# Optimization experiments

Hardware: AMD Instinct MI355X
Metric: run time of the kernel (lower is better)

## Reference

```python
import jax, jax.numpy as jnp
import numpy as np

N_NODES = 50000


def gcn_conv(x, W, b, row, col, n):
    """PyG GCNConv with default add_self_loops=True, normalize=True.
    out[i] = sum_{e: col[e]=i} d^-1/2[row[e]] d^-1/2[i] * (x@W)[row[e]]
             + d^-1[i]*(x@W)[i] + b,  where d = in-degree + 1 (self-loop).
    """
    x_lin = x @ W                                   # [n, out_ch]
    ones = jnp.ones(row.shape[0], dtype=x.dtype)
    deg = jax.ops.segment_sum(ones, col, num_segments=n) + 1.0  # self-loop
    dinv = jax.lax.rsqrt(deg)                       # deg >= 1, safe
    norm = dinv[row] * dinv[col]                    # [E]
    msg = norm[:, None] * x_lin[row]                # [E, out_ch]
    agg = jax.ops.segment_sum(msg, col, num_segments=n)
    self_term = (dinv * dinv)[:, None] * x_lin      # self-loop contribution
    return agg + self_term + b


def setup_inputs() -> dict:
    key = jax.random.key(0)
    ks = jax.random.split(key, 10)
    in_ch, hid, out_ch = 128, 256, 64
    E = 800000
    x = jax.random.normal(ks[0], (N_NODES, in_ch), dtype=jnp.float32)
    edge_attr = jax.random.normal(ks[1], (E, 8), dtype=jnp.float32)  # unused by forward
    edge_index = jax.random.randint(ks[2], (2, E), 0, N_NODES, dtype=jnp.int64)
    def glorot(k, fan_in, fan_out):
        s = float(np.sqrt(6.0 / (fan_in + fan_out)))
        return jax.random.uniform(k, (fan_in, fan_out), jnp.float32, -s, s)
    return {
        "x": x,
        "edge_attr": edge_attr,
        "edge_index": edge_index,
        "W1": glorot(ks[3], in_ch, hid), "b1": jnp.zeros((hid,), jnp.float32),
        "W2": glorot(ks[4], hid, hid),  "b2": jnp.zeros((hid,), jnp.float32),
        "W3": glorot(ks[5], hid, out_ch), "b3": jnp.zeros((out_ch,), jnp.float32),
    }


def reference(x, edge_attr, edge_index, W1, b1, W2, b2, W3, b3):
    n = x.shape[0]
    row, col = edge_index[0], edge_index[1]
    h = jax.nn.sigmoid(gcn_conv(x, W1, b1, row, col, n))
    h = jax.nn.sigmoid(gcn_conv(h, W2, b2, row, col, n))
    # dropout(p=0.1) in eval mode is identity
    return gcn_conv(h, W3, b3, row, col, n)
```

## Files before the change

### kernel.cpp

```cpp
#include <hip/hip_runtime.h>
#include <hip/hip_bf16.h>

typedef __bf16 bf16x8_t __attribute__((ext_vector_type(8)));
typedef float f32x4_t __attribute__((ext_vector_type(4)));

__device__ __forceinline__ float bits2f(unsigned int u) {
    union { unsigned int u; float f; } c; c.u = u; return c.f;
}
__device__ __forceinline__ unsigned short f2bf_bits(float f) {
    __hip_bfloat16 h = __float2bfloat16(f);
    return __builtin_bit_cast(unsigned short, h);
}

__global__ void sentinel_fill(float* __restrict__ out, int n) {
    int i = blockIdx.x * blockDim.x + threadIdx.x;
    if (i < n) out[i] = 100.0f;
}

__global__ void detect_ei(const unsigned int* __restrict__ ei, int* __restrict__ flags) {
    int lane = threadIdx.x;
    int cz = 0;
    #pragma unroll
    for (int j = 0; j < 4; ++j) {
        int idx = lane * 4 + j;
        cz += (ei[2 * idx + 1] == 0u);
    }
    #pragma unroll
    for (int off = 32; off; off >>= 1) cz += __shfl_down(cz, off);
    if (lane == 0) flags[0] = (cz > 200);
}


__global__ void count_rank_dual(const int* __restrict__ ei, int* __restrict__ cnt,
                                int* __restrict__ rank, int E, int M,
                                const int* __restrict__ flags) {
    int e = blockIdx.x * blockDim.x + threadIdx.x;
    if (e < E) {
        int c = flags[0] ? ei[2 * E + 2 * e] : ei[E + e];
        int rk = 0;
        if ((unsigned)c < (unsigned)M) rk = atomicAdd(&cnt[c], 1);
        rank[e] = rk;
    }
}

__global__ void scan_blocks(const int* __restrict__ cnt, int* __restrict__ excl,
                            int* __restrict__ bsum, int n) {
    int tid = threadIdx.x;
    int i = blockIdx.x * 256 + tid;
    int lane = tid & 63, wv = tid >> 6;
    __shared__ int ws[4];
    int v = (i < n) ? cnt[i] : 0;
    int s = v;
    #pragma unroll
    for (int off = 1; off < 64; off <<= 1) {
        int t = __shfl_up(s, off);
        if (lane >= off) s += t;
    }
    if (lane == 63) ws[wv] = s;
    __syncthreads();
    if (tid == 0) { int a = 0; for (int q = 0; q < 4; ++q) { int t = ws[q]; ws[q] = a; a += t; } }
    __syncthreads();
    int ex = s - v + ws[wv];
    if (i < n) excl[i] = ex;
    if (tid == 255) bsum[blockIdx.x] = ex + v;
}

__global__ void scan_bsums(const int* __restrict__ bsum, int* __restrict__ boff,
                           int nb, int* __restrict__ colptr, int n) {
    int tid = threadIdx.x, lane = tid & 63, wv = tid >> 6;
    __shared__ int ws[4];
    __shared__ int carry;
    if (tid == 0) carry = 0;
    __syncthreads();
    for (int base = 0; base < nb; base += 256) {
        int i = base + tid;
        int v = (i < nb) ? bsum[i] : 0;
        int s = v;
        #pragma unroll
        for (int off = 1; off < 64; off <<= 1) {
            int t = __shfl_up(s, off);
            if (lane >= off) s += t;
        }
        if (lane == 63) ws[wv] = s;
        __syncthreads();
        if (tid == 0) { int a = carry; for (int q = 0; q < 4; ++q) { int t = ws[q]; ws[q] = a; a += t; } carry = a; }
        __syncthreads();
        int ex = s - v + ws[wv];
        if (i < nb) boff[i] = ex;
        __syncthreads();
    }
    if (tid == 0) colptr[n] = carry;
}

__global__ void scan_add_dinv(const int* __restrict__ excl, const int* __restrict__ boff,
                              const int* __restrict__ cnt, int* __restrict__ colptr,
                              float* __restrict__ dinv, int n) {
    int i = blockIdx.x * 256 + threadIdx.x;
    if (i < n) {
        colptr[i] = excl[i] + boff[blockIdx.x];
        dinv[i] = rsqrtf((float)cnt[i] + 1.0f);
    }
}

__global__ void fill_csr_part(const int* __restrict__ ei, const int* __restrict__ colptr,
                              const int* __restrict__ rank, int* __restrict__ esrc,
                              int E, int M, int psz, const int* __restrict__ flags) {
    int part = blockIdx.x & 7;
    int e = (blockIdx.x >> 3) * 256 + threadIdx.x;
    int lo = part * psz;
    int hi = lo + psz; if (hi > M) hi = M;
    if (e < E) {
        int r, c;
        if (flags[0]) { r = ei[2 * e]; c = ei[2 * E + 2 * e]; }
        else          { r = ei[e];     c = ei[E + e]; }
        if (c >= lo && c < hi && (unsigned)r < (unsigned)M) {
            int p = colptr[c] + rank[e];
            if ((unsigned)p < (unsigned)E) esrc[p] = r;
        }
    }
}

__global__ void transpose_all(const float* __restrict__ W1, const float* __restrict__ W2,
                              const float* __restrict__ W3,
                              unsigned short* __restrict__ Wt1, unsigned short* __restrict__ Wt2,
                              unsigned short* __restrict__ Wt3) {
    int i = blockIdx.x * 256 + threadIdx.x;
    if (i < 32768) {
        int k = i >> 8, n = i & 255;
        Wt1[n * 128 + k] = f2bf_bits(W1[i]);
    } else if (i < 32768 + 65536) {
        int j = i - 32768;
        int k = j >> 8, n = j & 255;
        Wt2[n * 256 + k] = f2bf_bits(W2[j]);
    } else if (i < 114688) {
        int j = i - 98304;
        int k = j >> 6, n = j & 63;
        Wt3[n * 256 + k] = f2bf_bits(W3[j]);
    }
}

__global__ void prescale_x(const float* __restrict__ x, const float* __restrict__ dinv,
                           unsigned short* __restrict__ xs, int total) {
    int i = blockIdx.x * 256 + threadIdx.x;
    if (i < total) {
        int row = i >> 7;
        xs[i] = f2bf_bits(x[i] * dinv[row]);
    }
}

template<int K, int BN, int NTOT, int EPI>
__global__ __launch_bounds__(256) void gemm_tile(
    const __bf16* __restrict__ A,
    const unsigned short* __restrict__ Bt,
    const float* __restrict__ dinv,
    const float* __restrict__ bias,
    void* __restrict__ Y,
    int M)
{
    constexpr int KS = (K > 128) ? 128 : K;
    constexpr int KP = KS + 8;
    constexpr int NT = BN / 2 / 16;
    __shared__ unsigned short Bs[BN * KP];

    const int tid  = threadIdx.x;
    const int lane = tid & 63;
    const int wave = tid >> 6;
    const int wm   = wave >> 1;
    const int wn   = wave & 1;
    const int quad = lane >> 4;
    const int l16  = lane & 15;
    const int n0   = blockIdx.y * BN;

    int mrow[4];
#pragma unroll
    for (int mt = 0; mt < 4; ++mt) {
        int r = blockIdx.x * 128 + wm * 64 + mt * 16 + l16;
        mrow[mt] = (r < M) ? r : (M - 1);
    }

    f32x4_t acc[4][NT];
#pragma unroll
    for (int mt = 0; mt < 4; ++mt)
#pragma unroll
        for (int t = 0; t < NT; ++t) acc[mt][t] = (f32x4_t){0.f, 0.f, 0.f, 0.f};

    const unsigned short* BsW = &Bs[(wn * (BN / 2)) * KP];

    for (int kh = 0; kh < K; kh += KS) {
        constexpr int CH = BN * KS / 8;
        for (int idx = tid; idx < CH; idx += 256) {
            int n  = idx / (KS / 8);
            int k8 = idx - n * (KS / 8);
            uint4 v = *(const uint4*)(Bt + (size_t)(n0 + n) * K + kh + k8 * 8);
            *(uint4*)&Bs[n * KP + k8 * 8] = v;
        }
        __syncthreads();

#pragma unroll
        for (int kc = 0; kc < KS; kc += 32) {
            bf16x8_t a[4], b[NT];
#pragma unroll
            for (int mt = 0; mt < 4; ++mt)
                a[mt] = *(const bf16x8_t*)(A + (size_t)mrow[mt] * K + kh + kc + quad * 8);
#pragma unroll
            for (int t = 0; t < NT; ++t)
                b[t] = *(const bf16x8_t*)&BsW[(t * 16 + l16) * KP + kc + quad * 8];
#pragma unroll
            for (int mt = 0; mt < 4; ++mt)
#pragma unroll
                for (int t = 0; t < NT; ++t)
                    acc[mt][t] = __builtin_amdgcn_mfma_f32_16x16x32_bf16(a[mt], b[t], acc[mt][t], 0, 0, 0);
        }
        if (kh + KS < K) __syncthreads();
    }

    float bv[NT];
    if constexpr (EPI == 1) {
#pragma unroll
        for (int t = 0; t < NT; ++t)
            bv[t] = bias[n0 + wn * (BN / 2) + t * 16 + l16];
    }

#pragma unroll
    for (int mt = 0; mt < 4; ++mt) {
        int rowbase = blockIdx.x * 128 + wm * 64 + mt * 16 + quad * 4;
#pragma unroll
        for (int r = 0; r < 4; ++r) {
            int rrow = rowbase + r;
            if (rrow < M) {
                if constexpr (EPI == 0) {
                    float dv = dinv[rrow];
#pragma unroll
                    for (int t = 0; t < NT; ++t) {
                        int ccol = n0 + wn * (BN / 2) + t * 16 + l16;
                        ((__hip_bfloat16*)Y)[(size_t)rrow * NTOT + ccol] =
                            __float2bfloat16(acc[mt][t][r] * dv);
                    }
                } else if constexpr (EPI == 1) {
#pragma unroll
                    for (int t = 0; t < NT; ++t) {
                        int ccol = n0 + wn * (BN / 2) + t * 16 + l16;
                        float o = acc[mt][t][r] + bv[t];
                        o = 1.f / (1.f + __expf(-o));
                        ((__hip_bfloat16*)Y)[(size_t)rrow * NTOT + ccol] = __float2bfloat16(o);
                    }
                } else {
                    float dv = dinv[rrow];
#pragma unroll
                    for (int t = 0; t < NT; ++t) {
                        int ccol = n0 + wn * (BN / 2) + t * 16 + l16;
                        float o = acc[mt][t][r] * dv;
                        int pk = __builtin_amdgcn_cvt_pk_fp8_f32(o, o, 0, false);
                        ((unsigned char*)Y)[(size_t)rrow * NTOT + ccol] = (unsigned char)(pk & 0xff);
                    }
                }
            }
        }
    }
}

__global__ __launch_bounds__(256) void aggregate_fp8_256(
    const unsigned char* __restrict__ Y8,
    const int* __restrict__ colptr,
    const int* __restrict__ esrc,
    const float* __restrict__ dinv,
    const float* __restrict__ bias,
    unsigned short* __restrict__ H,
    int M, int Etot)
{
    const int lane = threadIdx.x & 63;
    const int wave = threadIdx.x >> 6;
    const int l = lane & 15;
    const int g = lane >> 4;
    int node = blockIdx.x * 4 + wave;
    if (node >= M) return;

    int s = colptr[node];
    int e = colptr[node + 1];
    if (s < 0) s = 0;
    if (e > Etot) e = Etot;
    if (e < s) e = s;

    const char* Yb = (const char*)Y8;
    const unsigned loff = (unsigned)(l * 16);

    float acc[16];
    #pragma unroll
    for (int k = 0; k < 16; ++k) acc[k] = 0.f;

    auto unpack = [&](uint4 u) {
        auto p0 = __builtin_amdgcn_cvt_pk_f32_fp8(u.x, false);
        auto p1 = __builtin_amdgcn_cvt_pk_f32_fp8(u.x, true);
        auto p2 = __builtin_amdgcn_cvt_pk_f32_fp8(u.y, false);
        auto p3 = __builtin_amdgcn_cvt_pk_f32_fp8(u.y, true);
        auto p4 = __builtin_amdgcn_cvt_pk_f32_fp8(u.z, false);
        auto p5 = __builtin_amdgcn_cvt_pk_f32_fp8(u.z, true);
        auto p6 = __builtin_amdgcn_cvt_pk_f32_fp8(u.w, false);
        auto p7 = __builtin_amdgcn_cvt_pk_f32_fp8(u.w, true);
        acc[0]  += p0[0]; acc[1]  += p0[1];
        acc[2]  += p1[0]; acc[3]  += p1[1];
        acc[4]  += p2[0]; acc[5]  += p2[1];
        acc[6]  += p3[0]; acc[7]  += p3[1];
        acc[8]  += p4[0]; acc[9]  += p4[1];
        acc[10] += p5[0]; acc[11] += p5[1];
        acc[12] += p6[0]; acc[13] += p6[1];
        acc[14] += p7[0]; acc[15] += p7[1];
    };

    for (int base = s; base < e; base += 64) {
        int n = e - base; if (n > 64) n = 64;
        unsigned myOff = 0;
        if (lane < n) myOff = (unsigned)esrc[base + lane] << 8;
        int j = 0;
        #pragma unroll 2
        for (; j + 4 <= n; j += 4) {
            unsigned off = __shfl(myOff, j + g) + loff;
            uint4 u = *(const uint4*)(Yb + off);
            unpack(u);
        }
        if (j < n) {
            unsigned off = __shfl(myOff, j + g) + loff;
            if (j + g < n) {
                uint4 u = *(const uint4*)(Yb + off);
                unpack(u);
            }
        }
    }
    if (g == 0) {
        uint4 u = *(const uint4*)(Yb + ((unsigned)node << 8) + loff);
        unpack(u);
    }
    #pragma unroll
    for (int off = 16; off < 64; off <<= 1) {
        #pragma unroll
        for (int k = 0; k < 16; ++k) acc[k] += __shfl_xor(acc[k], off);
    }

    if (g == 0) {
        float dv = dinv[node];
        float o[16];
        #pragma unroll
        for (int k = 0; k < 16; ++k) {
            o[k] = acc[k] * dv + bias[l * 16 + k];
            o[k] = 1.f / (1.f + __expf(-o[k]));
        }
        uint4 s0, s1;
        s0.x = (unsigned)f2bf_bits(o[0])  | ((unsigned)f2bf_bits(o[1])  << 16);
        s0.y = (unsigned)f2bf_bits(o[2])  | ((unsigned)f2bf_bits(o[3])  << 16);
        s0.z = (unsigned)f2bf_bits(o[4])  | ((unsigned)f2bf_bits(o[5])  << 16);
        s0.w = (unsigned)f2bf_bits(o[6])  | ((unsigned)f2bf_bits(o[7])  << 16);
        s1.x = (unsigned)f2bf_bits(o[8])  | ((unsigned)f2bf_bits(o[9])  << 16);
        s1.y = (unsigned)f2bf_bits(o[10]) | ((unsigned)f2bf_bits(o[11]) << 16);
        s1.z = (unsigned)f2bf_bits(o[12]) | ((unsigned)f2bf_bits(o[13]) << 16);
        s1.w = (unsigned)f2bf_bits(o[14]) | ((unsigned)f2bf_bits(o[15]) << 16);
        unsigned short* Hp = H + (size_t)node * 256 + l * 16;
        *(uint4*)Hp       = s0;
        *(uint4*)(Hp + 8) = s1;
    }
}

template<int C, bool SIG, bool OUTF32, bool HASB>
__global__ __launch_bounds__(256) void aggregate2(
    const unsigned short* __restrict__ Y,
    const int* __restrict__ colptr,
    const int* __restrict__ esrc,
    const float* __restrict__ dinv,
    const float* __restrict__ bias,
    void* __restrict__ H,
    int M, int Etot)
{
    constexpr int G   = C / 8;
    constexpr int EPW = 64 / G;
    const int lane = threadIdx.x & 63;
    const int wave = threadIdx.x >> 6;
    const int l = lane & (G - 1);
    const int g = lane / G;
    int node = blockIdx.x * 4 + wave;
    if (node >= M) return;

    int s = colptr[node];
    int e = colptr[node + 1];
    if (s < 0) s = 0;
    if (e > Etot) e = Etot;
    if (e < s) e = s;

    const char* Yb = (const char*)Y;
    const unsigned loff = (unsigned)(l * 16);

    float acc[8];
    #pragma unroll
    for (int k = 0; k < 8; ++k) acc[k] = 0.f;

    auto unpack = [&](uint4 u) {
        acc[0] += bits2f(u.x << 16);
        acc[1] += bits2f(u.x & 0xffff0000u);
        acc[2] += bits2f(u.y << 16);
        acc[3] += bits2f(u.y & 0xffff0000u);
        acc[4] += bits2f(u.z << 16);
        acc[5] += bits2f(u.z & 0xffff0000u);
        acc[6] += bits2f(u.w << 16);
        acc[7] += bits2f(u.w & 0xffff0000u);
    };

    for (int base = s; base < e; base += 64) {
        int n = e - base; if (n > 64) n = 64;
        unsigned myOff = 0;
        if (lane < n) myOff = (unsigned)esrc[base + lane] * (unsigned)(C * 2);
        int j = 0;
        #pragma unroll 2
        for (; j + EPW <= n; j += EPW) {
            unsigned off = __shfl(myOff, j + g) + loff;
            uint4 u = *(const uint4*)(Yb + off);
            unpack(u);
        }
        if (j < n) {
            unsigned off = __shfl(myOff, j + g) + loff;
            if (j + g < n) {
                uint4 u = *(const uint4*)(Yb + off);
                unpack(u);
            }
        }
    }
    if (g == 0) {
        unsigned off = (unsigned)node * (unsigned)(C * 2) + loff;
        uint4 u = *(const uint4*)(Yb + off);
        unpack(u);
    }
    #pragma unroll
    for (int off = G; off < 64; off <<= 1) {
        #pragma unroll
        for (int k = 0; k < 8; ++k) acc[k] += __shfl_xor(acc[k], off);
    }

    if (g == 0) {
        float dv = dinv[node];
        float o[8];
        #pragma unroll
        for (int k = 0; k < 8; ++k) {
            o[k] = acc[k] * dv;
            if (HASB) o[k] += bias[l * 8 + k];
            if (SIG) o[k] = 1.f / (1.f + __expf(-o[k]));
        }
        if constexpr (OUTF32) {
            float* Hp = (float*)H + (size_t)node * C + l * 8;
            *(float4*)Hp       = (float4){o[0], o[1], o[2], o[3]};
            *(float4*)(Hp + 4) = (float4){o[4], o[5], o[6], o[7]};
        } else {
            uint4 st;
            st.x = (unsigned)f2bf_bits(o[0]) | ((unsigned)f2bf_bits(o[1]) << 16);
            st.y = (unsigned)f2bf_bits(o[2]) | ((unsigned)f2bf_bits(o[3]) << 16);
            st.z = (unsigned)f2bf_bits(o[4]) | ((unsigned)f2bf_bits(o[5]) << 16);
            st.w = (unsigned)f2bf_bits(o[6]) | ((unsigned)f2bf_bits(o[7]) << 16);
            *(uint4*)((unsigned short*)H + (size_t)node * C + l * 8) = st;
        }
    }
}


extern "C" void kernel_launch(void* const* d_in, const int* in_sizes, int n_in,
                              void* d_out, int out_size, void* d_ws, size_t ws_size,
                              hipStream_t stream)
{
    int iEI = 2, iW1 = 3, iB1 = 4, iW2 = 5, iB2 = 6, iW3 = 7, iB3 = 8;
    if (n_in == 8) { iEI = 1; iW1 = 2; iB1 = 3; iW2 = 4; iB2 = 5; iW3 = 6; iB3 = 7; }

    const float* x  = (const float*)d_in[0];
    const int* ei   = (const int*)d_in[iEI];
    const float* W1 = (const float*)d_in[iW1];
    const float* b1 = (const float*)d_in[iB1];
    const float* W2 = (const float*)d_in[iW2];
    const float* b2 = (const float*)d_in[iB2];
    const float* W3 = (const float*)d_in[iW3];
    const float* b3 = (const float*)d_in[iB3];

    const int M = in_sizes[0] / 128;
    const int E = in_sizes[iEI] / 2;
    const int NB = (M + 255) / 256;
    const int PSZ = (M + 7) / 8;

    auto rnd = [](size_t b) { return (b + 255) & ~(size_t)255; };
    size_t needed = rnd(64 * 4)
                  + rnd((size_t)M * 4) * 2
                  + rnd((size_t)(M + 1) * 4)
                  + rnd((size_t)M * 4)
                  + rnd((size_t)(NB + 1) * 4) * 2
                  + rnd((size_t)E * 4) * 2
                  + rnd((size_t)256 * 128 * 2)
                  + rnd((size_t)256 * 256 * 2)
                  + rnd((size_t)64 * 256 * 2)
                  + rnd((size_t)M * 256 * 2) * 2;
    if (ws_size < needed) {
        sentinel_fill<<<(out_size + 255) / 256, 256, 0, stream>>>((float*)d_out, out_size);
        return;
    }

    char* p = (char*)d_ws;
    auto alloc = [&](size_t bytes) {
        char* r = p;
        p += (bytes + 255) & ~(size_t)255;
        return r;
    };
    int* flags  = (int*)alloc(64 * 4);
    float* dinv = (float*)alloc((size_t)M * 4);
    int* cnt    = (int*)alloc((size_t)M * 4);
    int* colptr = (int*)alloc((size_t)(M + 1) * 4);
    int* excl   = (int*)alloc((size_t)M * 4);
    int* bsum   = (int*)alloc((size_t)(NB + 1) * 4);
    int* boff   = (int*)alloc((size_t)(NB + 1) * 4);
    int* esrc   = (int*)alloc((size_t)E * 4);
    int* rank   = (int*)alloc((size_t)E * 4);
    unsigned short* Wt1 = (unsigned short*)alloc((size_t)256 * 128 * 2);
    unsigned short* Wt2 = (unsigned short*)alloc((size_t)256 * 256 * 2);
    unsigned short* Wt3 = (unsigned short*)alloc((size_t)64 * 256 * 2);
    __hip_bfloat16* ybuf = (__hip_bfloat16*)alloc((size_t)M * 256 * 2);
    __hip_bfloat16* hbuf = (__hip_bfloat16*)alloc((size_t)M * 256 * 2);

    unsigned short* xs = (unsigned short*)ybuf;
    unsigned short* xa = (unsigned short*)ybuf + (size_t)M * 128;
    unsigned char*  y8 = (unsigned char*)ybuf;

    detect_ei<<<1, 64, 0, stream>>>((const unsigned int*)ei, flags);

    hipMemsetAsync(cnt, 0, (size_t)M * 4, stream);
    count_rank_dual<<<(E + 255) / 256, 256, 0, stream>>>(ei, cnt, rank, E, M, flags);
    scan_blocks<<<NB, 256, 0, stream>>>(cnt, excl, bsum, M);
    scan_bsums<<<1, 256, 0, stream>>>(bsum, boff, NB, colptr, M);
    scan_add_dinv<<<NB, 256, 0, stream>>>(excl, boff, cnt, colptr, dinv, M);
    fill_csr_part<<<((E + 255) / 256) * 8, 256, 0, stream>>>(
        ei, colptr, rank, esrc, E, M, PSZ, flags);
    transpose_all<<<(114688 + 255) / 256, 256, 0, stream>>>(W1, W2, W3, Wt1, Wt2, Wt3);

    int gmb = (M + 127) / 128;
    int ga  = (M + 3) / 4;

    prescale_x<<<((M * 128) + 255) / 256, 256, 0, stream>>>(x, dinv, xs, M * 128);
    aggregate2<128, false, false, false><<<ga, 256, 0, stream>>>(
        xs, colptr, esrc, dinv, nullptr, xa, M, E);
    gemm_tile<128, 128, 256, 1><<<dim3(gmb, 2), 256, 0, stream>>>(
        (const __bf16*)xa, Wt1, dinv, b1, hbuf, M);
    gemm_tile<256, 128, 256, 2><<<dim3(gmb, 2), 256, 0, stream>>>(
        (const __bf16*)hbuf, Wt2, dinv, b2, y8, M);
    aggregate_fp8_256<<<ga, 256, 0, stream>>>(
        y8, colptr, esrc, dinv, b2, (unsigned short*)hbuf, M, E);
    gemm_tile<256, 64, 64, 0><<<dim3(gmb, 1), 256, 0, stream>>>(
        (const __bf16*)hbuf, Wt3, dinv, b3, ybuf, M);
    aggregate2<64, false, true, true><<<ga, 256, 0, stream>>>(
        (const unsigned short*)ybuf, colptr, esrc, dinv, b3, d_out, M, E);
}
```

Before: 347.8 us.

## Restructure aggregation kernels so each wave spans a full feature row per edge

```diff
diff --git a/kernel.cpp b/kernel.cpp
--- a/kernel.cpp
+++ b/kernel.cpp
@@ -3,6 +3,7 @@
 
 typedef __bf16 bf16x8_t __attribute__((ext_vector_type(8)));
 typedef float f32x4_t __attribute__((ext_vector_type(4)));
+typedef float f32x2_t __attribute__((ext_vector_type(2)));
 
 __device__ __forceinline__ float bits2f(unsigned int u) {
     union { unsigned int u; float f; } c; c.u = u; return c.f;
@@ -10,6 +11,9 @@
 __device__ __forceinline__ unsigned short f2bf_bits(float f) {
     __hip_bfloat16 h = __float2bfloat16(f);
     return __builtin_bit_cast(unsigned short, h);
+}
+__device__ __forceinline__ f32x2_t unpack_bf2(unsigned int u) {
+    return (f32x2_t){bits2f(u << 16), bits2f(u & 0xffff0000u)};
 }
 
 __global__ void sentinel_fill(float* __restrict__ out, int n) {
@@ -259,7 +263,7 @@
     }
 }
 
-__global__ __launch_bounds__(256) void aggregate_fp8_256(
+__global__ __launch_bounds__(256) void aggregate_fp8_v2(
     const unsigned char* __restrict__ Y8,
     const int* __restrict__ colptr,
     const int* __restrict__ esrc,
@@ -270,8 +274,6 @@
 {
     const int lane = threadIdx.x & 63;
     const int wave = threadIdx.x >> 6;
-    const int l = lane & 15;
-    const int g = lane >> 4;
     int node = blockIdx.x * 4 + wave;
     if (node >= M) return;
 
@@ -282,99 +284,49 @@
     if (e < s) e = s;
 
     const char* Yb = (const char*)Y8;
-    const unsigned loff = (unsigned)(l * 16);
-
-    float acc[16];
-    #pragma unroll
-    for (int k = 0; k < 16; ++k) acc[k] = 0.f;
-
-    auto unpack = [&](uint4 u) {
-        auto p0 = __builtin_amdgcn_cvt_pk_f32_fp8(u.x, false);
-        auto p1 = __builtin_amdgcn_cvt_pk_f32_fp8(u.x, true);
-        auto p2 = __builtin_amdgcn_cvt_pk_f32_fp8(u.y, false);
-        auto p3 = __builtin_amdgcn_cvt_pk_f32_fp8(u.y, true);
-        auto p4 = __builtin_amdgcn_cvt_pk_f32_fp8(u.z, false);
-        auto p5 = __builtin_amdgcn_cvt_pk_f32_fp8(u.z, true);
-        auto p6 = __builtin_amdgcn_cvt_pk_f32_fp8(u.w, false);
-        auto p7 = __builtin_amdgcn_cvt_pk_f32_fp8(u.w, true);
-        acc[0]  += p0[0]; acc[1]  += p0[1];
-        acc[2]  += p1[0]; acc[3]  += p1[1];
-        acc[4]  += p2[0]; acc[5]  += p2[1];
-        acc[6]  += p3[0]; acc[7]  += p3[1];
-        acc[8]  += p4[0]; acc[9]  += p4[1];
-        acc[10] += p5[0]; acc[11] += p5[1];
-        acc[12] += p6[0]; acc[13] += p6[1];
-        acc[14] += p7[0]; acc[15] += p7[1];
-    };
-
-    for (int base = s; base < e; base += 64) {
-        int n = e - base; if (n > 64) n = 64;
-        unsigned myOff = 0;
-        if (lane < n) myOff = (unsigned)esrc[base + lane] << 8;
-        int j = 0;
-        #pragma unroll 2
-        for (; j + 4 <= n; j += 4) {
-            unsigned off = __shfl(myOff, j + g) + loff;
-            uint4 u = *(const uint4*)(Yb + off);
-            unpack(u);
-        }
-        if (j < n) {
-            unsigned off = __shfl(myOff, j + g) + loff;
-            if (j + g < n) {
-                uint4 u = *(const uint4*)(Yb + off);
-                unpack(u);
-            }
-        }
-    }
-    if (g == 0) {
-        uint4 u = *(const uint4*)(Yb + ((unsigned)node << 8) + loff);
-        unpack(u);
-    }
-    #pragma unroll
-    for (int off = 16; off < 64; off <<= 1) {
-        #pragma unroll
-        for (int k = 0; k < 16; ++k) acc[k] += __shfl_xor(acc[k], off);
-    }
-
-    if (g == 0) {
-        float dv = dinv[node];
-        float o[16];
-        #pragma unroll
-        for (int k = 0; k < 16; ++k) {
-            o[k] = acc[k] * dv + bias[l * 16 + k];
-            o[k] = 1.f / (1.f + __expf(-o[k]));
-        }
-        uint4 s0, s1;
-        s0.x = (unsigned)f2bf_bits(o[0])  | ((unsigned)f2bf_bits(o[1])  << 16);
-        s0.y = (unsigned)f2bf_bits(o[2])  | ((unsigned)f2bf_bits(o[3])  << 16);
-        s0.z = (unsigned)f2bf_bits(o[4])  | ((unsigned)f2bf_bits(o[5])  << 16);
-        s0.w = (unsigned)f2bf_bits(o[6])  | ((unsigned)f2bf_bits(o[7])  << 16);
-        s1.x = (unsigned)f2bf_bits(o[8])  | ((unsigned)f2bf_bits(o[9])  << 16);
-        s1.y = (unsigned)f2bf_bits(o[10]) | ((unsigned)f2bf_bits(o[11]) << 16);
-        s1.z = (unsigned)f2bf_bits(o[12]) | ((unsigned)f2bf_bits(o[13]) << 16);
-        s1.w = (unsigned)f2bf_bits(o[14]) | ((unsigned)f2bf_bits(o[15]) << 16);
-        unsigned short* Hp = H + (size_t)node * 256 + l * 16;
-        *(uint4*)Hp       = s0;
-        *(uint4*)(Hp + 8) = s1;
-    }
-}
-
-template<int C, bool SIG, bool OUTF32, bool HASB>
-__global__ __launch_bounds__(256) void aggregate2(
-    const unsigned short* __restrict__ Y,
+    const unsigned lb = (unsigned)(lane * 4);
+
+    f32x2_t a0 = {0.f, 0.f}, a1 = {0.f, 0.f};
+
+    {
+        unsigned u = *(const unsigned*)(Yb + (((unsigned)node) << 8) + lb);
+        a0 += __builtin_amdgcn_cvt_pk_f32_fp8(u, false);
+        a1 += __builtin_amdgcn_cvt_pk_f32_fp8(u, true);
+    }
+#pragma unroll 4
+    for (int t = s; t < e; ++t) {
+        unsigned off = (((unsigned)esrc[t]) << 8) + lb;
+        unsigned u = *(const unsigned*)(Yb + off);
+        a0 += __builtin_amdgcn_cvt_pk_f32_fp8(u, false);
+        a1 += __builtin_amdgcn_cvt_pk_f32_fp8(u, true);
+    }
+
+    float dv = dinv[node];
+    float4 bv = *(const float4*)(bias + lane * 4);
+    float o0 = a0[0] * dv + bv.x;
+    float o1 = a0[1] * dv + bv.y;
+    float o2 = a1[0] * dv + bv.z;
+    float o3 = a1[1] * dv + bv.w;
+    o0 = 1.f / (1.f + __expf(-o0));
+    o1 = 1.f / (1.f + __expf(-o1));
+    o2 = 1.f / (1.f + __expf(-o2));
+    o3 = 1.f / (1.f + __expf(-o3));
+    uint2 st;
+    st.x = (unsigned)f2bf_bits(o0) | ((unsigned)f2bf_bits(o1) << 16);
+    st.y = (unsigned)f2bf_bits(o2) | ((unsigned)f2bf_bits(o3) << 16);
+    *(uint2*)(H + (size_t)node * 256 + lane * 4) = st;
+}
+
+__global__ __launch_bounds__(256) void aggregate_bf16_128_v2(
+    const unsigned short* __restrict__ Yin,
     const int* __restrict__ colptr,
     const int* __restrict__ esrc,
     const float* __restrict__ dinv,
-    const float* __restrict__ bias,
-    void* __restrict__ H,
+    unsigned short* __restrict__ Hout,
     int M, int Etot)
 {
-    constexpr int G   = C / 8;
-    constexpr int EPW = 64 / G;
     const int lane = threadIdx.x & 63;
     const int wave = threadIdx.x >> 6;
-    const int l = lane & (G - 1);
-    const int g = lane / G;
     int node = blockIdx.x * 4 + wave;
     if (node >= M) return;
 
@@ -384,75 +336,73 @@
     if (e > Etot) e = Etot;
     if (e < s) e = s;
 
-    const char* Yb = (const char*)Y;
-    const unsigned loff = (unsigned)(l * 16);
-
-    float acc[8];
-    #pragma unroll
-    for (int k = 0; k < 8; ++k) acc[k] = 0.f;
-
-    auto unpack = [&](uint4 u) {
-        acc[0] += bits2f(u.x << 16);
-        acc[1] += bits2f(u.x & 0xffff0000u);
-        acc[2] += bits2f(u.y << 16);
-        acc[3] += bits2f(u.y & 0xffff0000u);
-        acc[4] += bits2f(u.z << 16);
-        acc[5] += bits2f(u.z & 0xffff0000u);
-        acc[6] += bits2f(u.w << 16);
-        acc[7] += bits2f(u.w & 0xffff0000u);
-    };
-
-    for (int base = s; base < e; base += 64) {
-        int n = e - base; if (n > 64) n = 64;
-        unsigned myOff = 0;
-        if (lane < n) myOff = (unsigned)esrc[base + lane] * (unsigned)(C * 2);
-        int j = 0;
-        #pragma unroll 2
-        for (; j + EPW <= n; j += EPW) {
-            unsigned off = __shfl(myOff, j + g) + loff;
-            uint4 u = *(const uint4*)(Yb + off);
-            unpack(u);
-        }
-        if (j < n) {
-            unsigned off = __shfl(myOff, j + g) + loff;
-            if (j + g < n) {
-                uint4 u = *(const uint4*)(Yb + off);
-                unpack(u);
-            }
-        }
-    }
+    const char* Yb = (const char*)Yin;
+    const unsigned lb = (unsigned)(lane * 4);
+
+    f32x2_t a = {0.f, 0.f};
+    {
+        unsigned u = *(const unsigned*)(Yb + (((unsigned)node) << 8) + lb);
+        a += unpack_bf2(u);
+    }
+#pragma unroll 4
+    for (int t = s; t < e; ++t) {
+        unsigned off = (((unsigned)esrc[t]) << 8) + lb;
+        unsigned u = *(const unsigned*)(Yb + off);
+        a += unpack_bf2(u);
+    }
+
+    float dv = dinv[node];
+    unsigned st = (unsigned)f2bf_bits(a[0] * dv) | ((unsigned)f2bf_bits(a[1] * dv) << 16);
+    *(unsigned*)((char*)Hout + (size_t)node * 256 + lane * 4) = st;
+}
+
+__global__ __launch_bounds__(256) void aggregate_bf16_64_f32(
+    const unsigned short* __restrict__ Yin,
+    const int* __restrict__ colptr,
+    const int* __restrict__ esrc,
+    const float* __restrict__ dinv,
+    const float* __restrict__ bias,
+    float* __restrict__ out,
+    int M, int Etot)
+{
+    const int lane = threadIdx.x & 63;
+    const int wave = threadIdx.x >> 6;
+    const int l5 = lane & 31;
+    const int g  = lane >> 5;
+    int node = blockIdx.x * 4 + wave;
+    if (node >= M) return;
+
+    int s = colptr[node];
+    int e = colptr[node + 1];
+    if (s < 0) s = 0;
+    if (e > Etot) e = Etot;
+    if (e < s) e = s;
+
+    const char* Yb = (const char*)Yin;
+    const unsigned lb = (unsigned)(l5 * 4);
+
+    f32x2_t a = {0.f, 0.f};
     if (g == 0) {
-        unsigned off = (unsigned)node * (unsigned)(C * 2) + loff;
-        uint4 u = *(const uint4*)(Yb + off);
-        unpack(u);
-    }
-    #pragma unroll
-    for (int off = G; off < 64; off <<= 1) {
-        #pragma unroll
-        for (int k = 0; k < 8; ++k) acc[k] += __shfl_xor(acc[k], off);
-    }
+        unsigned u = *(const unsigned*)(Yb + (((unsigned)node) << 7) + lb);
+        a += unpack_bf2(u);
+    }
+#pragma unroll 4
+    for (int t = s + g; t < e; t += 2) {
+        unsigned off = (((unsigned)esrc[t]) << 7) + lb;
+        unsigned u = *(const unsigned*)(Yb + off);
+        a += unpack_bf2(u);
+    }
+
+    a[0] += __shfl_xor(a[0], 32);
+    a[1] += __shfl_xor(a[1], 32);
 
     if (g == 0) {
         float dv = dinv[node];
-        float o[8];
-        #pragma unroll
-        for (int k = 0; k < 8; ++k) {
-            o[k] = acc[k] * dv;
-            if (HASB) o[k] += bias[l * 8 + k];
-            if (SIG) o[k] = 1.f / (1.f + __expf(-o[k]));
-        }
-        if constexpr (OUTF32) {
-            float* Hp = (float*)H + (size_t)node * C + l * 8;
-            *(float4*)Hp       = (float4){o[0], o[1], o[2], o[3]};
-            *(float4*)(Hp + 4) = (float4){o[4], o[5], o[6], o[7]};
-        } else {
-            uint4 st;
-            st.x = (unsigned)f2bf_bits(o[0]) | ((unsigned)f2bf_bits(o[1]) << 16);
-            st.y = (unsigned)f2bf_bits(o[2]) | ((unsigned)f2bf_bits(o[3]) << 16);
-            st.z = (unsigned)f2bf_bits(o[4]) | ((unsigned)f2bf_bits(o[5]) << 16);
-            st.w = (unsigned)f2bf_bits(o[6]) | ((unsigned)f2bf_bits(o[7]) << 16);
-            *(uint4*)((unsigned short*)H + (size_t)node * C + l * 8) = st;
-        }
+        float2 bv = *(const float2*)(bias + l5 * 2);
+        float2 st;
+        st.x = a[0] * dv + bv.x;
+        st.y = a[1] * dv + bv.y;
+        *(float2*)(out + (size_t)node * 64 + l5 * 2) = st;
     }
 }
 
@@ -534,16 +484,16 @@
     int ga  = (M + 3) / 4;
 
     prescale_x<<<((M * 128) + 255) / 256, 256, 0, stream>>>(x, dinv, xs, M * 128);
-    aggregate2<128, false, false, false><<<ga, 256, 0, stream>>>(
-        xs, colptr, esrc, dinv, nullptr, xa, M, E);
+    aggregate_bf16_128_v2<<<ga, 256, 0, stream>>>(
+        xs, colptr, esrc, dinv, xa, M, E);
     gemm_tile<128, 128, 256, 1><<<dim3(gmb, 2), 256, 0, stream>>>(
         (const __bf16*)xa, Wt1, dinv, b1, hbuf, M);
     gemm_tile<256, 128, 256, 2><<<dim3(gmb, 2), 256, 0, stream>>>(
         (const __bf16*)hbuf, Wt2, dinv, b2, y8, M);
-    aggregate_fp8_256<<<ga, 256, 0, stream>>>(
+    aggregate_fp8_v2<<<ga, 256, 0, stream>>>(
         y8, colptr, esrc, dinv, b2, (unsigned short*)hbuf, M, E);
     gemm_tile<256, 64, 64, 0><<<dim3(gmb, 1), 256, 0, stream>>>(
         (const __bf16*)hbuf, Wt3, dinv, b3, ybuf, M);
-    aggregate2<64, false, true, true><<<ga, 256, 0, stream>>>(
-        (const unsigned short*)ybuf, colptr, esrc, dinv, b3, d_out, M, E);
-}
+    aggregate_bf16_64_f32<<<ga, 256, 0, stream>>>(
+        (const unsigned short*)ybuf, colptr, esrc, dinv, b3, (float*)d_out, M, E);
+}
```

After: 343.9 us. Within noise of the previous version (-1.1%).
